# Optimization experiments

Hardware: AMD Instinct MI355X
Metric: run time of the kernel (lower is better)

The kernel has to match this reference:

```python
import math
import jax, jax.numpy as jnp
import numpy as np

B, S, D, H = 2, 2048, 2048, 16
HD = D // H  # head_dim = 128, rotary_dim = HD (full rotation)
ROPE_BASE = 10000.0


def setup_inputs() -> dict:
    key = jax.random.key(0)
    k0, k1, k2 = jax.random.split(key, 3)
    return {
        "x": jax.random.normal(k0, (B, S, D), dtype=jnp.float32),
        "Wqkv": jax.random.normal(k1, (D, 3 * D), dtype=jnp.float32) * 0.02,
        "bqkv": jnp.zeros((3 * D,), dtype=jnp.float32),
        "Wout": jax.random.normal(k2, (D, D), dtype=jnp.float32) * 0.02,
        "bout": jnp.zeros((D,), dtype=jnp.float32),
    }


def _rope_cos_sin(seqlen, dim):
    # flash-attn RotaryEmbedding: inv_freq over even indices, outer with positions
    inv_freq = 1.0 / (ROPE_BASE ** (jnp.arange(0, dim, 2, dtype=jnp.float32) / dim))
    t = jnp.arange(seqlen, dtype=jnp.float32)
    freqs = jnp.outer(t, inv_freq)  # (S, dim/2)
    return jnp.cos(freqs), jnp.sin(freqs)


def reference(x, Wqkv, bqkv, Wout, bout):
    b, s, d = x.shape
    hd = d // H
    # fused QKV projection -> (B, S, 3, H, HD)
    qkv = (x @ Wqkv + bqkv).reshape(b, s, 3, H, hd)
    q, k, v = qkv[:, :, 0], qkv[:, :, 1], qkv[:, :, 2]  # (B,S,H,HD)

    cos, sin = _rope_cos_sin(s, hd)
    c = cos[:, None, :]  # (S,1,HD/2) broadcast over heads
    si = sin[:, None, :]

    def rot(t):
        # split-half rotary (as in apply_rotary_emb_qkv), computed in fp32
        t1, t2 = jnp.split(t.astype(jnp.float32), 2, axis=-1)
        return jnp.concatenate([t1 * c - t2 * si, t1 * si + t2 * c], axis=-1).astype(x.dtype)

    q = rot(q)
    k = rot(k)

    scale = 1.0 / math.sqrt(hd)
    scores = jnp.einsum("bthd,bshd->bhts", q, k * scale)  # (B,H,S,S)
    causal_mask = jnp.triu(jnp.full((s, s), -10000.0, dtype=scores.dtype), 1)
    attn = jax.nn.softmax(scores + causal_mask, axis=-1)
    ctx = jnp.einsum("bhts,bshd->bthd", attn, v).reshape(b, s, d)
    return ctx @ Wout + bout
```

## Files before the change

### kernel.cpp

```cpp
#include <hip/hip_runtime.h>
#include <hip/hip_bf16.h>

typedef __attribute__((ext_vector_type(4))) float fx4;
typedef __attribute__((ext_vector_type(8))) short bx8;
typedef __hip_bfloat16 bf16;

#define GLD16(dst, src)                                                        \
  __builtin_amdgcn_global_load_lds(                                            \
      (__attribute__((address_space(1))) void*)(src),                          \
      (__attribute__((address_space(3))) void*)(dst), 16, 0, 0)

__device__ inline float bf2f(short s_) {
  unsigned int u = ((unsigned int)(unsigned short)s_) << 16;
  float f;
  __builtin_memcpy(&f, &u, 4);
  return f;
}
__device__ inline short f2bf(float f) {
  __hip_bfloat16 h = __float2bfloat16(f);
  short r;
  __builtin_memcpy(&r, &h, 2);
  return r;
}

__global__ __launch_bounds__(256) void k_cast(const float* __restrict__ in,
                                              bf16* __restrict__ out, int n4) {
  int i = blockIdx.x * 256 + threadIdx.x;
  if (i >= n4) return;
  float4 v = reinterpret_cast<const float4*>(in)[i];
  bf16 t[4] = {__float2bfloat16(v.x), __float2bfloat16(v.y),
               __float2bfloat16(v.z), __float2bfloat16(v.w)};
  reinterpret_cast<ushort4*>(out)[i] = *reinterpret_cast<ushort4*>(t);
}

__global__ void k_tcast(const float* __restrict__ in, bf16* __restrict__ out,
                        int R, int C) {
  __shared__ float tile[32][33];
  int c0 = blockIdx.x * 32, r0 = blockIdx.y * 32;
  int tx = threadIdx.x, ty = threadIdx.y;
#pragma unroll
  for (int j = 0; j < 4; ++j)
    tile[ty + j * 8][tx] = in[(size_t)(r0 + ty + j * 8) * C + c0 + tx];
  __syncthreads();
#pragma unroll
  for (int j = 0; j < 4; ++j)
    out[(size_t)(c0 + ty + j * 8) * R + r0 + tx] =
        __float2bfloat16(tile[tx][ty + j * 8]);
}

__global__ __launch_bounds__(256) void k_ropetab(float* __restrict__ cosT,
                                                 float* __restrict__ sinT) {
  int idx = blockIdx.x * 256 + threadIdx.x;
  int t = idx >> 6, i = idx & 63;
  float inv = expf(-logf(10000.0f) * (float)i * (1.0f / 64.0f));
  float fr = (float)t * inv;
  cosT[idx] = cosf(fr);
  sinT[idx] = sinf(fr);
}

__global__ __launch_bounds__(256) void k_rope(bf16* __restrict__ qkv,
                                              const float* __restrict__ cosT,
                                              const float* __restrict__ sinT) {
  int t = blockIdx.x * 256 + threadIdx.x;
  int d0 = (t & 7) * 8;
  int qk = (t >> 3) & 1;
  int h = (t >> 4) & 15;
  int s = (t >> 8) & 2047;
  int b = (t >> 19) & 1;
  bf16* base = qkv + (size_t)(b * 2048 + s) * 6144 + qk * 2048 + h * 128;
  bx8 lo = *(const bx8*)(base + d0);
  bx8 hi = *(const bx8*)(base + 64 + d0);
  float4 ca = *(const float4*)&cosT[s * 64 + d0];
  float4 cb = *(const float4*)&cosT[s * 64 + d0 + 4];
  float4 sa = *(const float4*)&sinT[s * 64 + d0];
  float4 sb = *(const float4*)&sinT[s * 64 + d0 + 4];
  float c[8] = {ca.x, ca.y, ca.z, ca.w, cb.x, cb.y, cb.z, cb.w};
  float si[8] = {sa.x, sa.y, sa.z, sa.w, sb.x, sb.y, sb.z, sb.w};
  bx8 olo, ohi;
#pragma unroll
  for (int e = 0; e < 8; ++e) {
    float t1 = bf2f(lo[e]), t2 = bf2f(hi[e]);
    olo[e] = f2bf(t1 * c[e] - t2 * si[e]);
    ohi[e] = f2bf(t1 * si[e] + t2 * c[e]);
  }
  *(bx8*)(base + d0) = olo;
  *(bx8*)(base + 64 + d0) = ohi;
}

__global__ void k_vtrans(const bf16* __restrict__ qkv, bf16* __restrict__ vT) {
  __shared__ bf16 tile[32][33];
  int s0 = blockIdx.x * 32, d0 = blockIdx.y * 32, bh = blockIdx.z;
  int b = bh >> 4, h = bh & 15;
  int tx = threadIdx.x, ty = threadIdx.y;
#pragma unroll
  for (int j = 0; j < 4; ++j)
    tile[ty + j * 8][tx] =
        qkv[(size_t)(b * 2048 + s0 + ty + j * 8) * 6144 + 4096 + h * 128 + d0 + tx];
  __syncthreads();
#pragma unroll
  for (int j = 0; j < 4; ++j)
    vT[(size_t)(bh * 128 + d0 + ty + j * 8) * 2048 + s0 + tx] = tile[tx][ty + j * 8];
}

__global__ __launch_bounds__(512, 4) void k_gemm256(
    const bf16* __restrict__ A, const bf16* __restrict__ BT,
    const float* __restrict__ bias, void* __restrict__ Cp, int M, int N, int K,
    int NBX, int out_bf16) {
  __shared__ __align__(16) bf16 As[2][256 * 32];
  __shared__ __align__(16) bf16 Bs[2][128 * 32];
  const int tid = threadIdx.x;
  const int lane = tid & 63, wid = tid >> 6;
  const int lr = lane & 15, lg = lane >> 4;
  const int wr = wid >> 1, wc = wid & 1;
  const int nwg = gridDim.x, bid = blockIdx.x;
  const int swz = (bid & 7) * (nwg >> 3) + (bid >> 3);
  const int mb = swz / NBX, nb = swz - mb * NBX;
  const int m0 = mb * 256, n0 = nb * 128;
  const int NT = K >> 5;

  fx4 acc[4][4];
#pragma unroll
  for (int m = 0; m < 4; ++m)
#pragma unroll
    for (int n = 0; n < 4; ++n) acc[m][n] = (fx4)(0.0f);

  auto SA = [&](int buf, int t) {
#pragma unroll
    for (int q = 0; q < 2; ++q) {
      const int L = q * 512 + tid;
      const int row = L >> 2, u = L & 3;
      GLD16(&As[buf][L * 8],
            A + (size_t)(m0 + row) * K + t * 32 + ((u ^ ((row >> 1) & 3)) * 8));
    }
  };
  auto SB = [&](int buf, int t) {
    const int L = tid;
    const int row = L >> 2, u = L & 3;
    GLD16(&Bs[buf][L * 8],
          BT + (size_t)(n0 + row) * K + t * 32 + ((u ^ ((row >> 1) & 3)) * 8));
  };

  SA(0, 0); SB(0, 0);

  for (int t = 0; t < NT; ++t) {
    const int buf = t & 1;
    if (t + 1 < NT) {
      SA(buf ^ 1, t + 1); SB(buf ^ 1, t + 1);
      asm volatile("s_waitcnt vmcnt(3)" ::: "memory");
    } else {
      asm volatile("s_waitcnt vmcnt(0)" ::: "memory");
    }
    __builtin_amdgcn_s_barrier();

    bx8 af[4], bfr[4];
#pragma unroll
    for (int m = 0; m < 4; ++m) {
      const int r = wr * 64 + m * 16 + lr;
      af[m] = *(const bx8*)&As[buf][r * 32 + ((lg ^ ((r >> 1) & 3)) * 8)];
    }
#pragma unroll
    for (int n = 0; n < 4; ++n) {
      const int r = wc * 64 + n * 16 + lr;
      bfr[n] = *(const bx8*)&Bs[buf][r * 32 + ((lg ^ ((r >> 1) & 3)) * 8)];
    }
    asm volatile("s_waitcnt lgkmcnt(0)" ::: "memory");
    __builtin_amdgcn_sched_barrier(0);
    __builtin_amdgcn_s_setprio(1);
#pragma unroll
    for (int m = 0; m < 4; ++m)
#pragma unroll
      for (int n = 0; n < 4; ++n)
        acc[m][n] =
            __builtin_amdgcn_mfma_f32_16x16x32_bf16(af[m], bfr[n], acc[m][n], 0, 0, 0);
    __builtin_amdgcn_s_setprio(0);
    __builtin_amdgcn_s_barrier();
  }

  float bv[4];
#pragma unroll
  for (int n = 0; n < 4; ++n) bv[n] = bias[n0 + wc * 64 + n * 16 + lr];
#pragma unroll
  for (int m = 0; m < 4; ++m)
#pragma unroll
    for (int n = 0; n < 4; ++n) {
      const int col = n0 + wc * 64 + n * 16 + lr;
#pragma unroll
      for (int j = 0; j < 4; ++j) {
        const int row = m0 + wr * 64 + m * 16 + lg * 4 + j;
        const float v = acc[m][n][j] + bv[n];
        if (out_bf16)
          ((bf16*)Cp)[(size_t)row * N + col] = __float2bfloat16(v);
        else
          ((float*)Cp)[(size_t)row * N + col] = v;
      }
    }
}

#define ATT_SL2E 0.12751740f

__global__ __launch_bounds__(256, 2) void k_attn2(
    const bf16* __restrict__ qkv, const bf16* __restrict__ vT,
    bf16* __restrict__ ctx, float* __restrict__ O0, float* __restrict__ O1,
    float* __restrict__ l0, float* __restrict__ l1) {
  __shared__ __align__(16) bf16 Ks[2][128 * 128];
  __shared__ __align__(16) bf16 Ps[4][32 * 64];
  const int tid = threadIdx.x;
  const int lane = tid & 63, w = tid >> 6;
  const int lr = lane & 15, lg = lane >> 4;
  const int bid = blockIdx.x;
  const int u = bid >> 5, bh = bid & 31;
  const int b = bh >> 4, h = bh & 15;
  int qt, t0, t1;
  if (u < 8) {
    qt = 8 + u; t0 = 0; t1 = 8;
  } else if (u < 16) {
    qt = 23 - u; t0 = 8; t1 = qt + 1;
  } else {
    qt = 23 - u; t0 = 0; t1 = qt + 1;
  }
  const int single = (u >= 16);
  const int nt = t1 - t0;

  const bf16* kbase = qkv + (size_t)b * 2048 * 6144 + 2048 + h * 128;
  const bf16* vbase = vT + (size_t)(b * 16 + h) * 128 * 2048;

  auto STAGE = [&](int bufi, int kt) {
    const int kv0 = kt * 128;
#pragma unroll
    for (int q = 0; q < 8; ++q) {
      const int slot = q * 256 + tid;
      const int row = slot >> 4, uu = slot & 15;
      GLD16(&Ks[bufi][slot * 8],
            kbase + (size_t)(kv0 + row) * 6144 + ((uu ^ (row & 15)) * 8));
    }
  };

  const bf16* qbase =
      qkv + (size_t)(b * 2048 + qt * 128 + w * 32) * 6144 + h * 128;
  bx8 qf[2][4];
#pragma unroll
  for (int m = 0; m < 2; ++m)
#pragma unroll
    for (int ks = 0; ks < 4; ++ks)
      qf[m][ks] = *(const bx8*)(qbase + (size_t)(m * 16 + lr) * 6144 + ks * 32 + lg * 8);

  bx8 vones;
#pragma unroll
  for (int e = 0; e < 8; ++e) vones[e] = (short)0x3F80;

  fx4 oacc[2][8], lacc[2];
#pragma unroll
  for (int m = 0; m < 2; ++m) {
    lacc[m] = (fx4)(0.0f);
#pragma unroll
    for (int d = 0; d < 8; ++d) oacc[m][d] = (fx4)(0.0f);
  }

  const int qrow0 = qt * 128 + w * 32;

  STAGE(0, t0);
  for (int i = 0; i < nt; ++i) {
    const int kt = t0 + i;
    const int cur = i & 1;
    if (i + 1 < nt) {
      STAGE(cur ^ 1, kt + 1);
      asm volatile("s_waitcnt vmcnt(8)" ::: "memory");
    } else {
      asm volatile("s_waitcnt vmcnt(0)" ::: "memory");
    }
    __builtin_amdgcn_s_barrier();
    asm volatile("" ::: "memory");

#pragma unroll
    for (int h2 = 0; h2 < 2; ++h2) {
      const int kv0 = kt * 128 + h2 * 64;
      if (kv0 > qrow0 + 31) continue;

      fx4 sacc[2][4];
#pragma unroll
      for (int n = 0; n < 4; ++n) {
        sacc[0][n] = (fx4)(0.0f);
        sacc[1][n] = (fx4)(0.0f);
      }
      __builtin_amdgcn_s_setprio(1);
#pragma unroll
      for (int n = 0; n < 4; ++n) {
        const int r = h2 * 64 + n * 16 + lr;
#pragma unroll
        for (int ks = 0; ks < 4; ++ks) {
          const bx8 kf = *(const bx8*)&Ks[cur][r * 128 + (((ks * 4 + lg) ^ lr) * 8)];
          sacc[0][n] =
              __builtin_amdgcn_mfma_f32_16x16x32_bf16(qf[0][ks], kf, sacc[0][n], 0, 0, 0);
          sacc[1][n] =
              __builtin_amdgcn_mfma_f32_16x16x32_bf16(qf[1][ks], kf, sacc[1][n], 0, 0, 0);
        }
      }
      __builtin_amdgcn_s_setprio(0);

      const bool needmask = (kv0 + 63) > qrow0;
#pragma unroll
      for (int n = 0; n < 4; ++n) {
        const int kvi = kv0 + n * 16 + lr;
#pragma unroll
        for (int m = 0; m < 2; ++m)
#pragma unroll
          for (int j = 0; j < 4; ++j) {
            float v = sacc[m][n][j] * ATT_SL2E;
            if (needmask) {
              const int qi = qrow0 + m * 16 + lg * 4 + j;
              if (kvi > qi) v = -200.0f;
            }
            const float p = exp2f(fminf(v, 60.0f));
            const int r = m * 16 + lg * 4 + j, c = n * 16 + lr;
            const int c2 = (c & 7) | (((c >> 3) ^ (r & 7)) << 3);
            Ps[w][r * 64 + c2] = __float2bfloat16(p);
          }
      }

      __builtin_amdgcn_s_setprio(1);
#pragma unroll
      for (int ks2 = 0; ks2 < 2; ++ks2) {
        const int uu = ((ks2 * 4 + lg) ^ (lr & 7)) * 8;
        const bx8 pf0 = *(const bx8*)&Ps[w][(0 * 16 + lr) * 64 + uu];
        const bx8 pf1 = *(const bx8*)&Ps[w][(1 * 16 + lr) * 64 + uu];
        lacc[0] = __builtin_amdgcn_mfma_f32_16x16x32_bf16(pf0, vones, lacc[0], 0, 0, 0);
        lacc[1] = __builtin_amdgcn_mfma_f32_16x16x32_bf16(pf1, vones, lacc[1], 0, 0, 0);
#pragma unroll
        for (int dn = 0; dn < 8; ++dn) {
          const bx8 vf = *(const bx8*)(vbase + (size_t)(dn * 16 + lr) * 2048 + kv0 +
                                       ks2 * 32 + lg * 8);
          oacc[0][dn] =
              __builtin_amdgcn_mfma_f32_16x16x32_bf16(pf0, vf, oacc[0][dn], 0, 0, 0);
          oacc[1][dn] =
              __builtin_amdgcn_mfma_f32_16x16x32_bf16(pf1, vf, oacc[1][dn], 0, 0, 0);
        }
      }
      __builtin_amdgcn_s_setprio(0);
    }
    __builtin_amdgcn_s_barrier();
    asm volatile("" ::: "memory");
  }

  if (single) {
    float rl[2][4];
#pragma unroll
    for (int m = 0; m < 2; ++m)
#pragma unroll
      for (int j = 0; j < 4; ++j) rl[m][j] = 1.0f / lacc[m][j];
#pragma unroll
    for (int m = 0; m < 2; ++m)
#pragma unroll
      for (int dn = 0; dn < 8; ++dn)
#pragma unroll
        for (int j = 0; j < 4; ++j) {
          const int row = qt * 128 + w * 32 + m * 16 + lg * 4 + j;
          ctx[(size_t)(b * 2048 + row) * 2048 + h * 128 + dn * 16 + lr] =
              __float2bfloat16(oacc[m][dn][j] * rl[m][j]);
        }
  } else {
    float* Op = (u < 8) ? O0 : O1;
    float* lp = (u < 8) ? l0 : l1;
    float* obase =
        Op + (((size_t)(b * 16 + h)) * 1024 + (qt * 128 - 1024 + w * 32)) * 128;
#pragma unroll
    for (int m = 0; m < 2; ++m)
#pragma unroll
      for (int dn = 0; dn < 8; ++dn)
#pragma unroll
        for (int j = 0; j < 4; ++j)
          obase[(m * 16 + lg * 4 + j) * 128 + dn * 16 + lr] = oacc[m][dn][j];
    if (lr == 0) {
      float* lbase =
          lp + ((size_t)(b * 16 + h)) * 1024 + (qt * 128 - 1024 + w * 32);
#pragma unroll
      for (int m = 0; m < 2; ++m)
#pragma unroll
        for (int j = 0; j < 4; ++j) lbase[m * 16 + lg * 4 + j] = lacc[m][j];
    }
  }
}

__global__ __launch_bounds__(256) void k_comb(const float* __restrict__ O0,
                                              const float* __restrict__ O1,
                                              const float* __restrict__ l0,
                                              const float* __restrict__ l1,
                                              bf16* __restrict__ ctx) {
  const int idx = blockIdx.x * 256 + threadIdx.x;
  const size_t base = (size_t)idx * 8;
  const size_t rowi = base >> 7;
  const float rl = 1.0f / (l0[rowi] + l1[rowi]);
  const float4 a0 = *(const float4*)&O0[base];
  const float4 b0 = *(const float4*)&O0[base + 4];
  const float4 a1 = *(const float4*)&O1[base];
  const float4 b1 = *(const float4*)&O1[base + 4];
  const int d = (int)(base & 127);
  const int s = (int)(rowi & 1023);
  const int bh = (int)(rowi >> 10);
  const int b = bh >> 4, h = bh & 15;
  bf16 o[8] = {__float2bfloat16((a0.x + a1.x) * rl), __float2bfloat16((a0.y + a1.y) * rl),
               __float2bfloat16((a0.z + a1.z) * rl), __float2bfloat16((a0.w + a1.w) * rl),
               __float2bfloat16((b0.x + b1.x) * rl), __float2bfloat16((b0.y + b1.y) * rl),
               __float2bfloat16((b0.z + b1.z) * rl), __float2bfloat16((b0.w + b1.w) * rl)};
  bf16* p = ctx + (size_t)(b * 2048 + 1024 + s) * 2048 + h * 128 + d;
  *(ushort4*)p = *(ushort4*)o;
  *(ushort4*)(p + 4) = *(ushort4*)(o + 4);
}

extern "C" void kernel_launch(void* const* d_in, const int* in_sizes, int n_in,
                              void* d_out, int out_size, void* d_ws, size_t ws_size,
                              hipStream_t stream) {
  const float* x = (const float*)d_in[0];
  const float* Wqkv = (const float*)d_in[1];
  const float* bqkv = (const float*)d_in[2];
  const float* Wout = (const float*)d_in[3];
  const float* bout = (const float*)d_in[4];
  float* out = (float*)d_out;

  char* ws = (char*)d_ws;
  bf16* xb    = (bf16*)(ws + 0);
  bf16* wqkvT = (bf16*)(ws + 16777216);
  bf16* woutT = (bf16*)(ws + 41943040);
  bf16* qkvb  = (bf16*)(ws + 50331648);
  bf16* vTb   = (bf16*)(ws + 100663296);
  bf16* ctxb  = (bf16*)(ws + 117440512);
  float* cosT = (float*)(ws + 134217728);
  float* sinT = (float*)(ws + 134742016);
  float* O0 = (float*)(ws + 0);
  float* O1 = (float*)(ws + 16777216);
  float* l0 = (float*)(ws + 33554432);
  float* l1 = (float*)(ws + 33685504);

  k_cast<<<8192, 256, 0, stream>>>(x, xb, 2097152);
  k_tcast<<<dim3(192, 64), dim3(32, 8), 0, stream>>>(Wqkv, wqkvT, 2048, 6144);
  k_tcast<<<dim3(64, 64), dim3(32, 8), 0, stream>>>(Wout, woutT, 2048, 2048);
  k_ropetab<<<512, 256, 0, stream>>>(cosT, sinT);
  k_gemm256<<<768, 512, 0, stream>>>(xb, wqkvT, bqkv, qkvb, 4096, 6144, 2048, 48, 1);
  k_rope<<<4096, 256, 0, stream>>>(qkvb, cosT, sinT);
  k_vtrans<<<dim3(64, 4, 32), dim3(32, 8), 0, stream>>>(qkvb, vTb);
  k_attn2<<<768, 256, 0, stream>>>(qkvb, vTb, ctxb, O0, O1, l0, l1);
  k_comb<<<2048, 256, 0, stream>>>(O0, O1, l0, l1, ctxb);
  k_gemm256<<<256, 512, 0, stream>>>(ctxb, woutT, bout, out, 4096, 2048, 2048, 16, 0);
}
```

Before: 347.7 us.

## Replace pipelined 256x128 GEMM with simple 128x128 GEMM; halve attention KV tile

The GEMM kernel drops the double-buffered, XCD-swizzled 256x128 tile with a BK=32 pipeline. In its place is a simpler single-buffered 128x128 tile with BK=64, a 2D grid and __syncthreads between stages, which gives up the overlap of loads with MFMA work. The attention kernel now stages 64-row K tiles instead of 128-row ones, halving its LDS use, and raises the occupancy hint to 3 blocks per CU. The tile ranges and wait counts are adjusted to match. The aim is more resident workgroups, with the risk of losing latency hiding in the GEMM.

```diff
diff --git a/kernel.cpp b/kernel.cpp
--- a/kernel.cpp
+++ b/kernel.cpp
@@ -102,21 +102,17 @@
     vT[(size_t)(bh * 128 + d0 + ty + j * 8) * 2048 + s0 + tx] = tile[tx][ty + j * 8];
 }
 
-__global__ __launch_bounds__(512, 4) void k_gemm256(
+__global__ __launch_bounds__(256) void k_gemm_bt(
     const bf16* __restrict__ A, const bf16* __restrict__ BT,
     const float* __restrict__ bias, void* __restrict__ Cp, int M, int N, int K,
-    int NBX, int out_bf16) {
-  __shared__ __align__(16) bf16 As[2][256 * 32];
-  __shared__ __align__(16) bf16 Bs[2][128 * 32];
+    int out_bf16) {
+  __shared__ __align__(16) bf16 As[128 * 64];
+  __shared__ __align__(16) bf16 Bs[128 * 64];
   const int tid = threadIdx.x;
-  const int lane = tid & 63, wid = tid >> 6;
+  const int m0 = blockIdx.y * 128, n0 = blockIdx.x * 128;
+  const int lane = tid & 63, w = tid >> 6;
   const int lr = lane & 15, lg = lane >> 4;
-  const int wr = wid >> 1, wc = wid & 1;
-  const int nwg = gridDim.x, bid = blockIdx.x;
-  const int swz = (bid & 7) * (nwg >> 3) + (bid >> 3);
-  const int mb = swz / NBX, nb = swz - mb * NBX;
-  const int m0 = mb * 256, n0 = nb * 128;
-  const int NT = K >> 5;
+  const int wr = w >> 1, wc = w & 1;
 
   fx4 acc[4][4];
 #pragma unroll
@@ -124,61 +120,45 @@
 #pragma unroll
     for (int n = 0; n < 4; ++n) acc[m][n] = (fx4)(0.0f);
 
-  auto SA = [&](int buf, int t) {
-#pragma unroll
-    for (int q = 0; q < 2; ++q) {
-      const int L = q * 512 + tid;
-      const int row = L >> 2, u = L & 3;
-      GLD16(&As[buf][L * 8],
-            A + (size_t)(m0 + row) * K + t * 32 + ((u ^ ((row >> 1) & 3)) * 8));
-    }
-  };
-  auto SB = [&](int buf, int t) {
-    const int L = tid;
-    const int row = L >> 2, u = L & 3;
-    GLD16(&Bs[buf][L * 8],
-          BT + (size_t)(n0 + row) * K + t * 32 + ((u ^ ((row >> 1) & 3)) * 8));
-  };
-
-  SA(0, 0); SB(0, 0);
-
-  for (int t = 0; t < NT; ++t) {
-    const int buf = t & 1;
-    if (t + 1 < NT) {
-      SA(buf ^ 1, t + 1); SB(buf ^ 1, t + 1);
-      asm volatile("s_waitcnt vmcnt(3)" ::: "memory");
-    } else {
-      asm volatile("s_waitcnt vmcnt(0)" ::: "memory");
-    }
-    __builtin_amdgcn_s_barrier();
-
-    bx8 af[4], bfr[4];
-#pragma unroll
-    for (int m = 0; m < 4; ++m) {
-      const int r = wr * 64 + m * 16 + lr;
-      af[m] = *(const bx8*)&As[buf][r * 32 + ((lg ^ ((r >> 1) & 3)) * 8)];
-    }
-#pragma unroll
-    for (int n = 0; n < 4; ++n) {
-      const int r = wc * 64 + n * 16 + lr;
-      bfr[n] = *(const bx8*)&Bs[buf][r * 32 + ((lg ^ ((r >> 1) & 3)) * 8)];
-    }
-    asm volatile("s_waitcnt lgkmcnt(0)" ::: "memory");
-    __builtin_amdgcn_sched_barrier(0);
-    __builtin_amdgcn_s_setprio(1);
-#pragma unroll
-    for (int m = 0; m < 4; ++m)
-#pragma unroll
-      for (int n = 0; n < 4; ++n)
-        acc[m][n] =
-            __builtin_amdgcn_mfma_f32_16x16x32_bf16(af[m], bfr[n], acc[m][n], 0, 0, 0);
-    __builtin_amdgcn_s_setprio(0);
-    __builtin_amdgcn_s_barrier();
+  for (int kt = 0; kt < K; kt += 64) {
+#pragma unroll
+    for (int q = 0; q < 4; ++q) {
+      const int slot = q * 256 + tid;
+      const int row = slot >> 3, u = slot & 7;
+      const int us = (u ^ (row & 7)) * 8;
+      GLD16(&As[slot * 8], A + (size_t)(m0 + row) * K + kt + us);
+      GLD16(&Bs[slot * 8], BT + (size_t)(n0 + row) * K + kt + us);
+    }
+    __syncthreads();
+#pragma unroll
+    for (int ks = 0; ks < 2; ++ks) {
+      bx8 af[4], bf[4];
+#pragma unroll
+      for (int m = 0; m < 4; ++m) {
+        const int r = wr * 64 + m * 16 + lr;
+        const int u = ((ks * 4 + lg) ^ (lr & 7)) * 8;
+        af[m] = *(const bx8*)&As[r * 64 + u];
+      }
+#pragma unroll
+      for (int n = 0; n < 4; ++n) {
+        const int r = wc * 64 + n * 16 + lr;
+        const int u = ((ks * 4 + lg) ^ (lr & 7)) * 8;
+        bf[n] = *(const bx8*)&Bs[r * 64 + u];
+      }
+#pragma unroll
+      for (int m = 0; m < 4; ++m)
+#pragma unroll
+        for (int n = 0; n < 4; ++n)
+          acc[m][n] =
+              __builtin_amdgcn_mfma_f32_16x16x32_bf16(af[m], bf[n], acc[m][n], 0, 0, 0);
+    }
+    __syncthreads();
   }
 
   float bv[4];
 #pragma unroll
   for (int n = 0; n < 4; ++n) bv[n] = bias[n0 + wc * 64 + n * 16 + lr];
+
 #pragma unroll
   for (int m = 0; m < 4; ++m)
 #pragma unroll
@@ -198,11 +178,11 @@
 
 #define ATT_SL2E 0.12751740f
 
-__global__ __launch_bounds__(256, 2) void k_attn2(
+__global__ __launch_bounds__(256, 3) void k_attn2(
     const bf16* __restrict__ qkv, const bf16* __restrict__ vT,
     bf16* __restrict__ ctx, float* __restrict__ O0, float* __restrict__ O1,
     float* __restrict__ l0, float* __restrict__ l1) {
-  __shared__ __align__(16) bf16 Ks[2][128 * 128];
+  __shared__ __align__(16) bf16 Ks[2][64 * 128];
   __shared__ __align__(16) bf16 Ps[4][32 * 64];
   const int tid = threadIdx.x;
   const int lane = tid & 63, w = tid >> 6;
@@ -212,11 +192,11 @@
   const int b = bh >> 4, h = bh & 15;
   int qt, t0, t1;
   if (u < 8) {
-    qt = 8 + u; t0 = 0; t1 = 8;
+    qt = 8 + u; t0 = 0; t1 = 16;
   } else if (u < 16) {
-    qt = 23 - u; t0 = 8; t1 = qt + 1;
+    qt = 23 - u; t0 = 16; t1 = 2 * qt + 2;
   } else {
-    qt = 23 - u; t0 = 0; t1 = qt + 1;
+    qt = 23 - u; t0 = 0; t1 = 2 * qt + 2;
   }
   const int single = (u >= 16);
   const int nt = t1 - t0;
@@ -225,9 +205,9 @@
   const bf16* vbase = vT + (size_t)(b * 16 + h) * 128 * 2048;
 
   auto STAGE = [&](int bufi, int kt) {
-    const int kv0 = kt * 128;
-#pragma unroll
-    for (int q = 0; q < 8; ++q) {
+    const int kv0 = kt * 64;
+#pragma unroll
+    for (int q = 0; q < 4; ++q) {
       const int slot = q * 256 + tid;
       const int row = slot >> 4, uu = slot & 15;
       GLD16(&Ks[bufi][slot * 8],
@@ -264,18 +244,15 @@
     const int cur = i & 1;
     if (i + 1 < nt) {
       STAGE(cur ^ 1, kt + 1);
-      asm volatile("s_waitcnt vmcnt(8)" ::: "memory");
+      asm volatile("s_waitcnt vmcnt(4)" ::: "memory");
     } else {
       asm volatile("s_waitcnt vmcnt(0)" ::: "memory");
     }
     __builtin_amdgcn_s_barrier();
     asm volatile("" ::: "memory");
 
-#pragma unroll
-    for (int h2 = 0; h2 < 2; ++h2) {
-      const int kv0 = kt * 128 + h2 * 64;
-      if (kv0 > qrow0 + 31) continue;
-
+    const int kv0 = kt * 64;
+    if (kv0 <= qrow0 + 31) {
       fx4 sacc[2][4];
 #pragma unroll
       for (int n = 0; n < 4; ++n) {
@@ -285,7 +262,7 @@
       __builtin_amdgcn_s_setprio(1);
 #pragma unroll
       for (int n = 0; n < 4; ++n) {
-        const int r = h2 * 64 + n * 16 + lr;
+        const int r = n * 16 + lr;
 #pragma unroll
         for (int ks = 0; ks < 4; ++ks) {
           const bx8 kf = *(const bx8*)&Ks[cur][r * 128 + (((ks * 4 + lg) ^ lr) * 8)];
@@ -434,10 +411,12 @@
   k_tcast<<<dim3(192, 64), dim3(32, 8), 0, stream>>>(Wqkv, wqkvT, 2048, 6144);
   k_tcast<<<dim3(64, 64), dim3(32, 8), 0, stream>>>(Wout, woutT, 2048, 2048);
   k_ropetab<<<512, 256, 0, stream>>>(cosT, sinT);
-  k_gemm256<<<768, 512, 0, stream>>>(xb, wqkvT, bqkv, qkvb, 4096, 6144, 2048, 48, 1);
+  k_gemm_bt<<<dim3(48, 32), 256, 0, stream>>>(xb, wqkvT, bqkv, qkvb, 4096, 6144,
+                                              2048, 1);
   k_rope<<<4096, 256, 0, stream>>>(qkvb, cosT, sinT);
   k_vtrans<<<dim3(64, 4, 32), dim3(32, 8), 0, stream>>>(qkvb, vTb);
   k_attn2<<<768, 256, 0, stream>>>(qkvb, vTb, ctxb, O0, O1, l0, l1);
   k_comb<<<2048, 256, 0, stream>>>(O0, O1, l0, l1, ctxb);
-  k_gemm256<<<256, 512, 0, stream>>>(ctxb, woutT, bout, out, 4096, 2048, 2048, 16, 0);
-}
+  k_gemm_bt<<<dim3(16, 32), 256, 0, stream>>>(ctxb, woutT, bout, out, 4096, 2048,
+                                              2048, 0);
+}
```

Measured after the change: 522.5 us. 1.5x slower.
